# Kernel tuning notes

Measured on AMD Instinct MI355X. Metric: run time of the kernel, lower is better.

Reference implementation:

```python
import jax, jax.numpy as jnp
import numpy as np

B, S, D = 2, 1024, 1024
H = 4 * D          # SwiGLU hidden
E = 8              # routed experts
K = 2              # top_k
NS = 1             # shared experts


def setup_inputs() -> dict:
    key = jax.random.key(0)
    ks = jax.random.split(key, 8)
    sc = 0.02  # init scale for stability
    return {
        "x": jax.random.normal(ks[0], (B, S, D), jnp.float32),
        "shared_w1": jax.random.normal(ks[1], (NS, D, H), jnp.float32) * sc,
        "shared_w2": jax.random.normal(ks[2], (NS, D, H), jnp.float32) * sc,
        "shared_w3": jax.random.normal(ks[3], (NS, H, D), jnp.float32) * sc,
        "w1": jax.random.normal(ks[4], (E, D, H), jnp.float32) * sc,
        "w2": jax.random.normal(ks[5], (E, D, H), jnp.float32) * sc,
        "w3": jax.random.normal(ks[6], (E, H, D), jnp.float32) * sc,
        "router_w": jax.random.normal(ks[7], (E, D), jnp.float32) * sc,
    }


def _experts(xf, W1, W2, W3):
    # xf: [T, D]; W1,W2: [E, D, H]; W3: [E, H, D] -> [E, T, D]
    h = jax.nn.silu(jnp.einsum("td,edh->eth", xf, W1)) * jnp.einsum("td,edh->eth", xf, W2)
    return jnp.einsum("eth,ehd->etd", h, W3)


def reference(x, shared_w1, shared_w2, shared_w3, w1, w2, w3, router_w):
    b, s, d = x.shape
    xf = x.reshape(-1, d)                       # [T, D]
    T = xf.shape[0]

    # shared experts (summed over NS experts)
    shared_out = _experts(xf, shared_w1, shared_w2, shared_w3).sum(axis=0)  # [T, D]

    # router: nn.Linear(dim, E, bias=False) => x @ W^T
    logits = jnp.einsum("td,ed->te", xf, router_w)   # [T, E]
    probs = jax.nn.softmax(logits, axis=1)
    topw, topi = jax.lax.top_k(probs, K)             # [T, K]
    topw = topw / topw.sum(axis=-1, keepdims=True)

    # dense combine-weight matrix [T, E]: zero except at selected experts
    cw = jnp.zeros((T, E), x.dtype).at[jnp.arange(T)[:, None], topi].add(topw)

    # all-expert outputs, weighted combine (faithful to masked loop + scatter-add)
    y = _experts(xf, w1, w2, w3)                     # [E, T, D]
    routed = jnp.einsum("te,etd->td", cw, y)         # [T, D]

    out = (shared_out + routed).reshape(b, s, d)
    return (out, logits)
```

## Files before the change

kernel.cpp:

```cpp
#include <hip/hip_runtime.h>


#define TD 2048
#define DD 1024
#define HH 4096
#define NEXP 8

typedef _Float16 f16x8 __attribute__((ext_vector_type(8)));
typedef _Float16 f16x4 __attribute__((ext_vector_type(4)));
typedef float f32x4 __attribute__((ext_vector_type(4)));

#define WS_COUNTS   0
#define WS_CURS     64
#define WS_HBASE    128
#define WS_TOKLIST  256
#define WS_TOPI     65792
#define WS_TOPW     82176
#define WS_POS      98560
#define WS_XH       131072
#define WS_H        4325376
#define WS_WT       63045632
#define WTSLOT      ((size_t)DD * HH)

typedef __attribute__((address_space(3))) void lds_void;
typedef const __attribute__((address_space(1))) void gbl_void;
__device__ __forceinline__ void gld16(void* l, const void* g) {
  __builtin_amdgcn_global_load_lds((gbl_void*)g, (lds_void*)l, 16, 0, 0);
}

__device__ __forceinline__ f16x8 frag_ld(const _Float16* tile, int r, int qsel) {
  int q = qsel ^ ((r >> 1) & 3);
  return *(const f16x8*)((const char*)tile + r * 64 + q * 16);
}

__global__ __launch_bounds__(256) void k_xh(const float* __restrict__ x, _Float16* __restrict__ xh) {
  int i = (blockIdx.x * 256 + threadIdx.x) * 8;
  float4 a = *(const float4*)(x + i), b = *(const float4*)(x + i + 4);
  f16x8 v = {(_Float16)a.x, (_Float16)a.y, (_Float16)a.z, (_Float16)a.w,
             (_Float16)b.x, (_Float16)b.y, (_Float16)b.z, (_Float16)b.w};
  *(f16x8*)(xh + i) = v;
}

__global__ __launch_bounds__(256) void k_router(const float* __restrict__ x,
    const float* __restrict__ rw, float* __restrict__ logits,
    int* __restrict__ topi, float* __restrict__ topw, int* __restrict__ counts) {
  int wv = threadIdx.x >> 6, lane = threadIdx.x & 63;
  int t = blockIdx.x * 4 + wv;
  const float* xt = x + (size_t)t * DD;
  float lg[NEXP];
#pragma unroll
  for (int e = 0; e < NEXP; ++e) {
    const float* we = rw + e * DD;
    float acc = 0.f;
#pragma unroll
    for (int j = 0; j < DD / 64; ++j) acc += xt[j * 64 + lane] * we[j * 64 + lane];
#pragma unroll
    for (int off = 32; off; off >>= 1) acc += __shfl_xor(acc, off);
    lg[e] = acc;
  }
  if (lane == 0) {
    float m = lg[0];
#pragma unroll
    for (int e = 1; e < NEXP; ++e) m = fmaxf(m, lg[e]);
    float p[NEXP];
#pragma unroll
    for (int e = 0; e < NEXP; ++e) p[e] = __expf(lg[e] - m);
    int i0 = 0; float p0 = p[0];
#pragma unroll
    for (int e = 1; e < NEXP; ++e) if (p[e] > p0) { p0 = p[e]; i0 = e; }
    int i1 = -1; float p1 = -1.f;
#pragma unroll
    for (int e = 0; e < NEXP; ++e) if (e != i0 && p[e] > p1) { p1 = p[e]; i1 = e; }
    float wsum = p0 + p1;
#pragma unroll
    for (int e = 0; e < NEXP; ++e) logits[t * NEXP + e] = lg[e];
    topi[t * 2] = i0; topi[t * 2 + 1] = i1;
    topw[t * 2] = p0 / wsum; topw[t * 2 + 1] = p1 / wsum;
    atomicAdd(&counts[i0], 1); atomicAdd(&counts[i1], 1);
  }
}

__global__ void k_offsets(const int* __restrict__ counts, int* __restrict__ hbase) {
  if (threadIdx.x == 0) {
    int base = TD;
    for (int e = 0; e < NEXP; ++e) { hbase[e] = base; base += (counts[e] + 127) & ~127; }
  }
}

__global__ void k_scatter(const int* __restrict__ topi, int* __restrict__ curs,
                          int* __restrict__ tokl, int* __restrict__ posarr) {
  int tid = blockIdx.x * 256 + threadIdx.x;
  if (tid >= TD * 2) return;
  int e = topi[tid];
  int pos = atomicAdd(&curs[e], 1);
  tokl[e * TD + pos] = tid >> 1;
  posarr[tid] = pos;
}

__device__ __forceinline__ void transpose_tile(const float* __restrict__ src,
    _Float16* __restrict__ dst, int R, int C, int r0, int c0) {
  __shared__ _Float16 tile[128][68];
  int t = threadIdx.x;
#pragma unroll
  for (int i = 0; i < 8; ++i) {
    int r = (t >> 4) + i * 16;
    int c = (t & 15) * 4;
    float4 v = *(const float4*)(src + (size_t)(r0 + r) * C + c0 + c);
    *(f16x4*)&tile[r][c] = (f16x4){(_Float16)v.x, (_Float16)v.y, (_Float16)v.z, (_Float16)v.w};
  }
  __syncthreads();
#pragma unroll
  for (int i = 0; i < 4; ++i) {
    int cc = (t >> 4) + i * 16;
    int rr = (t & 15) * 8;
    f16x8 hv;
#pragma unroll
    for (int j = 0; j < 8; ++j) hv[j] = tile[rr + j][cc];
    *(f16x8*)(dst + (size_t)(c0 + cc) * R + r0 + rr) = hv;
  }
}

__global__ __launch_bounds__(256) void k_tr1(const float* __restrict__ sw1, const float* __restrict__ sw2,
    const float* __restrict__ w1, const float* __restrict__ w2, _Float16* __restrict__ wt) {
  int id = blockIdx.y;
  const float* src = (id == 0) ? sw1 : (id == 1) ? sw2
                   : (id < 10) ? w1 + (size_t)(id - 2) * DD * HH
                               : w2 + (size_t)(id - 10) * DD * HH;
  _Float16* dst = wt + (size_t)id * WTSLOT;
  transpose_tile(src, dst, DD, HH, (blockIdx.x >> 6) * 128, (blockIdx.x & 63) * 64);
}

__global__ __launch_bounds__(256) void k_tr2(const float* __restrict__ sw3,
    const float* __restrict__ w3, _Float16* __restrict__ wt) {
  int id = blockIdx.y;
  const float* src = (id == 0) ? sw3 : w3 + (size_t)(id - 1) * HH * DD;
  _Float16* dst = wt + (size_t)id * WTSLOT;
  transpose_tile(src, dst, HH, DD, (blockIdx.x >> 4) * 128, (blockIdx.x & 15) * 64);
}

__global__ __launch_bounds__(256, 2) void k_gemm1(
    const _Float16* __restrict__ xh, const _Float16* __restrict__ wt,
    const int* __restrict__ counts, const int* __restrict__ hbase,
    const int* __restrict__ tok_list, _Float16* __restrict__ h) {
  __shared__ _Float16 lA[2][128 * 32];
  __shared__ _Float16 lB1[2][128 * 32];
  __shared__ _Float16 lB2[2][128 * 32];
  __shared__ int stok[128];

  int slot = blockIdx.y;
  const _Float16 *w1t, *w2t;
  int hrow0;
  if (slot < 16) {
    w1t = wt; w2t = wt + WTSLOT; hrow0 = slot * 128;
  } else {
    int e = (slot - 16) >> 4, rt = (slot - 16) & 15;
    if (rt * 128 >= counts[e]) return;
    w1t = wt + (size_t)(2 + e) * WTSLOT;
    w2t = wt + (size_t)(10 + e) * WTSLOT;
    hrow0 = hbase[e] + rt * 128;
  }
  if (threadIdx.x < 128) {
    int tok = (slot < 16) ? (hrow0 + threadIdx.x)
                          : tok_list[((slot - 16) >> 4) * TD + ((slot - 16) & 15) * 128 + threadIdx.x];
    stok[threadIdx.x] = tok;
  }
  __syncthreads();

  int n0 = blockIdx.x * 128;
  int wv = threadIdx.x >> 6, lane = threadIdx.x & 63;
  int wm = (wv & 1) * 64, wn = (wv >> 1) * 64;
  int qsel = lane >> 4;
  int r15 = lane & 15;

  const _Float16 *gA[2], *gB1[2], *gB2[2];
  int ldsoff[2];
#pragma unroll
  for (int jj = 0; jj < 2; ++jj) {
    int j = wv * 2 + jj;
    int n = j * 16 + (lane >> 2);
    int q = (lane & 3) ^ ((n >> 1) & 3);
    gA[jj]  = xh + (size_t)stok[n] * DD + q * 8;
    gB1[jj] = w1t + (size_t)(n0 + n) * DD + q * 8;
    gB2[jj] = w2t + (size_t)(n0 + n) * DD + q * 8;
    ldsoff[jj] = j * 1024 + lane * 16;
  }

#pragma unroll
  for (int jj = 0; jj < 2; ++jj) {
    gld16((char*)lA[0] + ldsoff[jj], gA[jj]);
    gld16((char*)lB1[0] + ldsoff[jj], gB1[jj]);
    gld16((char*)lB2[0] + ldsoff[jj], gB2[jj]);
  }

  f32x4 acc1[4][4] = {}; f32x4 acc2[4][4] = {};

  auto compute = [&](int b) {
    f16x8 af[4];
#pragma unroll
    for (int mi = 0; mi < 4; ++mi) af[mi] = frag_ld(lA[b], wm + mi * 16 + r15, qsel);
#pragma unroll
    for (int ni = 0; ni < 4; ++ni) {
      f16x8 b1 = frag_ld(lB1[b], wn + ni * 16 + r15, qsel);
      f16x8 b2 = frag_ld(lB2[b], wn + ni * 16 + r15, qsel);
#pragma unroll
      for (int mi = 0; mi < 4; ++mi) {
        acc1[mi][ni] = __builtin_amdgcn_mfma_f32_16x16x32_f16(af[mi], b1, acc1[mi][ni], 0, 0, 0);
        acc2[mi][ni] = __builtin_amdgcn_mfma_f32_16x16x32_f16(af[mi], b2, acc2[mi][ni], 0, 0, 0);
      }
    }
  };

  int cur = 0;
  __syncthreads();
  for (int kk = 32; kk < DD; kk += 32) {
#pragma unroll
    for (int jj = 0; jj < 2; ++jj) {
      gld16((char*)lA[cur ^ 1] + ldsoff[jj], gA[jj] + kk);
      gld16((char*)lB1[cur ^ 1] + ldsoff[jj], gB1[jj] + kk);
      gld16((char*)lB2[cur ^ 1] + ldsoff[jj], gB2[jj] + kk);
    }
    compute(cur);
    __syncthreads();
    cur ^= 1;
  }
  compute(cur);

#pragma unroll
  for (int mi = 0; mi < 4; ++mi)
#pragma unroll
    for (int ni = 0; ni < 4; ++ni)
#pragma unroll
      for (int i = 0; i < 4; ++i) {
        int r = wm + mi * 16 + (lane >> 4) * 4 + i;
        int c = wn + ni * 16 + (lane & 15);
        float a = acc1[mi][ni][i], b = acc2[mi][ni][i];
        h[(size_t)(hrow0 + r) * HH + n0 + c] = (_Float16)((a / (1.f + __expf(-a))) * b);
      }
}

__global__ __launch_bounds__(256, 2) void k_gemm2(
    const _Float16* __restrict__ h, const _Float16* __restrict__ wt,
    const int* __restrict__ counts, const int* __restrict__ hbase,
    _Float16* __restrict__ y0, _Float16* __restrict__ y1) {
  __shared__ _Float16 lA[2][128 * 32];
  __shared__ _Float16 lB[2][128 * 32];

  int slot = blockIdx.y;
  const _Float16* w3t;
  int hrow0;
  if (slot < 16) {
    w3t = wt; hrow0 = slot * 128;
  } else {
    int e = (slot - 16) >> 4, rt = (slot - 16) & 15;
    if (rt * 128 >= counts[e]) return;
    w3t = wt + (size_t)(1 + e) * WTSLOT;
    hrow0 = hbase[e] + rt * 128;
  }
  _Float16* y = blockIdx.z ? y1 : y0;
  int kz0 = blockIdx.z * (HH / 2);

  int n0 = blockIdx.x * 128;
  int wv = threadIdx.x >> 6, lane = threadIdx.x & 63;
  int wm = (wv & 1) * 64, wn = (wv >> 1) * 64;
  int qsel = lane >> 4;
  int r15 = lane & 15;

  const _Float16 *gA[2], *gB[2];
  int ldsoff[2];
#pragma unroll
  for (int jj = 0; jj < 2; ++jj) {
    int j = wv * 2 + jj;
    int n = j * 16 + (lane >> 2);
    int q = (lane & 3) ^ ((n >> 1) & 3);
    gA[jj] = h   + (size_t)(hrow0 + n) * HH + kz0 + q * 8;
    gB[jj] = w3t + (size_t)(n0 + n)   * HH + kz0 + q * 8;
    ldsoff[jj] = j * 1024 + lane * 16;
  }

#pragma unroll
  for (int jj = 0; jj < 2; ++jj) {
    gld16((char*)lA[0] + ldsoff[jj], gA[jj]);
    gld16((char*)lB[0] + ldsoff[jj], gB[jj]);
  }

  f32x4 acc[4][4] = {};

  auto compute = [&](int b) {
    f16x8 af[4];
#pragma unroll
    for (int mi = 0; mi < 4; ++mi) af[mi] = frag_ld(lA[b], wm + mi * 16 + r15, qsel);
#pragma unroll
    for (int ni = 0; ni < 4; ++ni) {
      f16x8 bf = frag_ld(lB[b], wn + ni * 16 + r15, qsel);
#pragma unroll
      for (int mi = 0; mi < 4; ++mi)
        acc[mi][ni] = __builtin_amdgcn_mfma_f32_16x16x32_f16(af[mi], bf, acc[mi][ni], 0, 0, 0);
    }
  };

  int cur = 0;
  __syncthreads();
  for (int kk = 32; kk < HH / 2; kk += 32) {
#pragma unroll
    for (int jj = 0; jj < 2; ++jj) {
      gld16((char*)lA[cur ^ 1] + ldsoff[jj], gA[jj] + kk);
      gld16((char*)lB[cur ^ 1] + ldsoff[jj], gB[jj] + kk);
    }
    compute(cur);
    __syncthreads();
    cur ^= 1;
  }
  compute(cur);

#pragma unroll
  for (int mi = 0; mi < 4; ++mi)
#pragma unroll
    for (int ni = 0; ni < 4; ++ni)
#pragma unroll
      for (int i = 0; i < 4; ++i) {
        int r = wm + mi * 16 + (lane >> 4) * 4 + i;
        int c = wn + ni * 16 + (lane & 15);
        y[(size_t)(hrow0 + r) * DD + n0 + c] = (_Float16)acc[mi][ni][i];
      }
}

__global__ __launch_bounds__(256) void k_combine(
    const _Float16* __restrict__ y0, const _Float16* __restrict__ y1,
    const int* __restrict__ topi, const float* __restrict__ topw,
    const int* __restrict__ posarr, const int* __restrict__ hbase,
    float* __restrict__ out) {
  int t = blockIdx.x;
  int c = threadIdx.x * 4;
  int e0 = topi[2 * t], e1 = topi[2 * t + 1];
  float w0 = topw[2 * t], w1 = topw[2 * t + 1];
  size_t rs = (size_t)t * DD + c;
  size_t r0 = (size_t)(hbase[e0] + posarr[2 * t]) * DD + c;
  size_t r1 = (size_t)(hbase[e1] + posarr[2 * t + 1]) * DD + c;
  f16x4 s0 = *(const f16x4*)(y0 + rs), s1 = *(const f16x4*)(y1 + rs);
  f16x4 a0 = *(const f16x4*)(y0 + r0), a1 = *(const f16x4*)(y1 + r0);
  f16x4 b0 = *(const f16x4*)(y0 + r1), b1 = *(const f16x4*)(y1 + r1);
  float4 o;
  float* op = &o.x;
#pragma unroll
  for (int i = 0; i < 4; ++i)
    op[i] = (float)s0[i] + (float)s1[i] + w0 * ((float)a0[i] + (float)a1[i])
          + w1 * ((float)b0[i] + (float)b1[i]);
  *(float4*)(out + rs) = o;
}

extern "C" void kernel_launch(void* const* d_in, const int* in_sizes, int n_in,
                              void* d_out, int out_size, void* d_ws, size_t ws_size,
                              hipStream_t stream) {
  const float* x   = (const float*)d_in[0];
  const float* sw1 = (const float*)d_in[1];
  const float* sw2 = (const float*)d_in[2];
  const float* sw3 = (const float*)d_in[3];
  const float* w1  = (const float*)d_in[4];
  const float* w2  = (const float*)d_in[5];
  const float* w3  = (const float*)d_in[6];
  const float* rw  = (const float*)d_in[7];
  float* out = (float*)d_out;
  char* ws = (char*)d_ws;

  int*   counts = (int*)(ws + WS_COUNTS);
  int*   curs   = (int*)(ws + WS_CURS);
  int*   hbase  = (int*)(ws + WS_HBASE);
  int*   tokl   = (int*)(ws + WS_TOKLIST);
  int*   topi   = (int*)(ws + WS_TOPI);
  float* topw   = (float*)(ws + WS_TOPW);
  int*   posarr = (int*)(ws + WS_POS);
  _Float16* xh   = (_Float16*)(ws + WS_XH);
  _Float16* hbuf = (_Float16*)(ws + WS_H);
  _Float16* wt   = (_Float16*)(ws + WS_WT);
  _Float16* ybuf0 = wt + 9 * WTSLOT;
  _Float16* ybuf1 = wt + 11 * WTSLOT;

  hipMemsetAsync(ws, 0, 65792, stream);

  k_xh<<<TD * DD / 2048, 256, 0, stream>>>(x, xh);
  k_router<<<TD / 4, 256, 0, stream>>>(x, rw, out + (size_t)TD * DD, topi, topw, counts);
  k_offsets<<<1, 64, 0, stream>>>(counts, hbase);
  k_scatter<<<16, 256, 0, stream>>>(topi, curs, tokl, posarr);

  k_tr1<<<dim3(512, 18), 256, 0, stream>>>(sw1, sw2, w1, w2, wt);
  k_gemm1<<<dim3(HH / 128, 144), 256, 0, stream>>>(xh, wt, counts, hbase, tokl, hbuf);
  k_tr2<<<dim3(512, 9), 256, 0, stream>>>(sw3, w3, wt);
  k_gemm2<<<dim3(DD / 128, 144, 2), 256, 0, stream>>>(hbuf, wt, counts, hbase, ybuf0, ybuf1);
  k_combine<<<TD, 256, 0, stream>>>(ybuf0, ybuf1, topi, topw, posarr, hbase, out);
}
```

Measured before the change: 818.5 us.

## Deepen LDS prefetch pipelines in both expert GEMMs with explicit vmcnt waits

Gate/up GEMM moves from double to triple buffering, and down-projection GEMM to four-stage buffering. Each uses s_waitcnt vmcnt with partial counts so several tile loads stay in flight while the current tile is computed. The aim is to hide global-to-LDS load latency that the previous two-buffer scheme with __syncthreads exposed. The cost is more LDS per block (gemm1 grows to 72KB and gemm2 to 64KB), which may reduce occupancy below the requested 2 blocks per CU. The hand-counted vmcnt values are fragile if the compiler emits a different number of loads.

```diff
diff --git a/kernel.cpp b/kernel.cpp
--- a/kernel.cpp
+++ b/kernel.cpp
@@ -142,9 +142,9 @@
     const _Float16* __restrict__ xh, const _Float16* __restrict__ wt,
     const int* __restrict__ counts, const int* __restrict__ hbase,
     const int* __restrict__ tok_list, _Float16* __restrict__ h) {
-  __shared__ _Float16 lA[2][128 * 32];
-  __shared__ _Float16 lB1[2][128 * 32];
-  __shared__ _Float16 lB2[2][128 * 32];
+  __shared__ _Float16 lA[3][128 * 32];
+  __shared__ _Float16 lB1[3][128 * 32];
+  __shared__ _Float16 lB2[3][128 * 32];
   __shared__ int stok[128];
 
   int slot = blockIdx.y;
@@ -185,12 +185,15 @@
     ldsoff[jj] = j * 1024 + lane * 16;
   }
 
-#pragma unroll
-  for (int jj = 0; jj < 2; ++jj) {
-    gld16((char*)lA[0] + ldsoff[jj], gA[jj]);
-    gld16((char*)lB1[0] + ldsoff[jj], gB1[jj]);
-    gld16((char*)lB2[0] + ldsoff[jj], gB2[jj]);
-  }
+#define G1_STAGE(buf, kk)                                   \
+  do {                                                      \
+    _Pragma("unroll")                                       \
+    for (int jj = 0; jj < 2; ++jj) {                        \
+      gld16((char*)lA[buf] + ldsoff[jj], gA[jj] + (kk));    \
+      gld16((char*)lB1[buf] + ldsoff[jj], gB1[jj] + (kk));  \
+      gld16((char*)lB2[buf] + ldsoff[jj], gB2[jj] + (kk));  \
+    }                                                       \
+  } while (0)
 
   f32x4 acc1[4][4] = {}; f32x4 acc2[4][4] = {};
 
@@ -210,20 +213,30 @@
     }
   };
 
-  int cur = 0;
-  __syncthreads();
-  for (int kk = 32; kk < DD; kk += 32) {
-#pragma unroll
-    for (int jj = 0; jj < 2; ++jj) {
-      gld16((char*)lA[cur ^ 1] + ldsoff[jj], gA[jj] + kk);
-      gld16((char*)lB1[cur ^ 1] + ldsoff[jj], gB1[jj] + kk);
-      gld16((char*)lB2[cur ^ 1] + ldsoff[jj], gB2[jj] + kk);
-    }
-    compute(cur);
-    __syncthreads();
-    cur ^= 1;
-  }
-  compute(cur);
+  G1_STAGE(0, 0);
+  G1_STAGE(1, 32);
+
+  int cb = 0, wb = 2;
+  for (int t = 0; t < DD / 32 - 2; ++t) {
+    G1_STAGE(wb, (t + 2) * 32);
+    asm volatile("s_waitcnt vmcnt(12)" ::: "memory");
+    __builtin_amdgcn_s_barrier();
+    compute(cb);
+    asm volatile("s_waitcnt lgkmcnt(0)" ::: "memory");
+    __builtin_amdgcn_s_barrier();
+    cb = (cb == 2) ? 0 : cb + 1;
+    wb = (wb == 2) ? 0 : wb + 1;
+  }
+  asm volatile("s_waitcnt vmcnt(6)" ::: "memory");
+  __builtin_amdgcn_s_barrier();
+  compute(cb);
+  asm volatile("s_waitcnt lgkmcnt(0)" ::: "memory");
+  __builtin_amdgcn_s_barrier();
+  cb = (cb == 2) ? 0 : cb + 1;
+  asm volatile("s_waitcnt vmcnt(0)" ::: "memory");
+  __builtin_amdgcn_s_barrier();
+  compute(cb);
+#undef G1_STAGE
 
 #pragma unroll
   for (int mi = 0; mi < 4; ++mi)
@@ -242,8 +255,8 @@
     const _Float16* __restrict__ h, const _Float16* __restrict__ wt,
     const int* __restrict__ counts, const int* __restrict__ hbase,
     _Float16* __restrict__ y0, _Float16* __restrict__ y1) {
-  __shared__ _Float16 lA[2][128 * 32];
-  __shared__ _Float16 lB[2][128 * 32];
+  __shared__ _Float16 lA[4][128 * 32];
+  __shared__ _Float16 lB[4][128 * 32];
 
   int slot = blockIdx.y;
   const _Float16* w3t;
@@ -277,11 +290,14 @@
     ldsoff[jj] = j * 1024 + lane * 16;
   }
 
-#pragma unroll
-  for (int jj = 0; jj < 2; ++jj) {
-    gld16((char*)lA[0] + ldsoff[jj], gA[jj]);
-    gld16((char*)lB[0] + ldsoff[jj], gB[jj]);
-  }
+#define G2_STAGE(buf, kk)                                 \
+  do {                                                    \
+    _Pragma("unroll")                                     \
+    for (int jj = 0; jj < 2; ++jj) {                      \
+      gld16((char*)lA[buf] + ldsoff[jj], gA[jj] + (kk));  \
+      gld16((char*)lB[buf] + ldsoff[jj], gB[jj] + (kk));  \
+    }                                                     \
+  } while (0)
 
   f32x4 acc[4][4] = {};
 
@@ -298,19 +314,33 @@
     }
   };
 
-  int cur = 0;
-  __syncthreads();
-  for (int kk = 32; kk < HH / 2; kk += 32) {
-#pragma unroll
-    for (int jj = 0; jj < 2; ++jj) {
-      gld16((char*)lA[cur ^ 1] + ldsoff[jj], gA[jj] + kk);
-      gld16((char*)lB[cur ^ 1] + ldsoff[jj], gB[jj] + kk);
-    }
-    compute(cur);
-    __syncthreads();
-    cur ^= 1;
-  }
-  compute(cur);
+  G2_STAGE(0, 0);
+  G2_STAGE(1, 32);
+  G2_STAGE(2, 64);
+
+  const int NT = (HH / 2) / 32;
+  for (int t = 0; t < NT - 3; ++t) {
+    G2_STAGE((t + 3) & 3, (t + 3) * 32);
+    asm volatile("s_waitcnt vmcnt(12)" ::: "memory");
+    __builtin_amdgcn_s_barrier();
+    compute(t & 3);
+    asm volatile("s_waitcnt lgkmcnt(0)" ::: "memory");
+    __builtin_amdgcn_s_barrier();
+  }
+  asm volatile("s_waitcnt vmcnt(8)" ::: "memory");
+  __builtin_amdgcn_s_barrier();
+  compute(61 & 3);
+  asm volatile("s_waitcnt lgkmcnt(0)" ::: "memory");
+  __builtin_amdgcn_s_barrier();
+  asm volatile("s_waitcnt vmcnt(4)" ::: "memory");
+  __builtin_amdgcn_s_barrier();
+  compute(62 & 3);
+  asm volatile("s_waitcnt lgkmcnt(0)" ::: "memory");
+  __builtin_amdgcn_s_barrier();
+  asm volatile("s_waitcnt vmcnt(0)" ::: "memory");
+  __builtin_amdgcn_s_barrier();
+  compute(63 & 3);
+#undef G2_STAGE
 
 #pragma unroll
   for (int mi = 0; mi < 4; ++mi)
```

Result: no change. 820.3 us (+0.2%).
